# Kernel tuning notes

Hardware: AMD Instinct MI355X
Metric: run time of the kernel (lower is better)

Reference implementation:

```python
import jax, jax.numpy as jnp
import numpy as np

N_NODES = 50000
N_EDGES = 800000
N_GRAPHS = 64
IN_DIM = 128
HID = 128
S, C = 4, 16
DIM1 = 3 * S * S  # 48
OUT_DIM = DIM1 * C  # 768


def gcn_conv(x, W, b, src, dst, w):
    """PyG GCNConv: linear transform, then sym-normalized aggregation with self-loops (weight 1)."""
    n = x.shape[0]
    h = x @ W  # [N, out]
    deg = jnp.zeros((n,), x.dtype).at[dst].add(w) + 1.0  # self-loop weight 1
    dinv = jax.lax.rsqrt(deg)
    norm = dinv[src] * w * dinv[dst]  # [E]
    agg = jnp.zeros_like(h).at[dst].add(h[src] * norm[:, None])
    agg = agg + h * (1.0 / deg)[:, None]  # self-loop messages
    return agg + b


def setup_inputs() -> dict:
    key = jax.random.key(0)
    ks = jax.random.split(key, 16)
    x = jax.random.normal(ks[0], (N_NODES, IN_DIM), jnp.float32)
    edge_index = jax.random.randint(ks[1], (2, N_EDGES), 0, N_NODES, jnp.int64)
    edge_attr = jax.random.uniform(ks[2], (N_EDGES,), jnp.float32)
    batch = jnp.sort(jax.random.randint(ks[3], (N_NODES,), 0, N_GRAPHS, jnp.int64))

    def glorot(k, fan_in, fan_out):
        s = np.sqrt(6.0 / (fan_in + fan_out)).astype(np.float32)
        return jax.random.uniform(k, (fan_in, fan_out), jnp.float32, -s, s)

    return {
        "x": x, "edge_index": edge_index, "edge_attr": edge_attr, "batch": batch,
        "W1": glorot(ks[4], IN_DIM, HID), "b1": jnp.zeros((HID,), jnp.float32),
        "W2": glorot(ks[5], HID, HID // 2), "b2": jnp.zeros((HID // 2,), jnp.float32),
        "W3": glorot(ks[6], HID // 2, HID // 4), "b3": jnp.zeros((HID // 4,), jnp.float32),
        "Wl": glorot(ks[7], HID // 4, OUT_DIM), "bl": jnp.zeros((OUT_DIM,), jnp.float32),
    }


def reference(x, edge_index, edge_attr, batch, W1, b1, W2, b2, W3, b3, Wl, bl):
    src, dst = edge_index[0], edge_index[1]
    w = edge_attr / edge_attr.max()
    h = jax.nn.relu(gcn_conv(x, W1, b1, src, dst, w))
    h = jax.nn.relu(gcn_conv(h, W2, b2, src, dst, w))
    h = jax.nn.relu(gcn_conv(h, W3, b3, src, dst, w))
    # global mean pool over graphs
    sums = jax.ops.segment_sum(h, batch, num_segments=N_GRAPHS)
    cnt = jax.ops.segment_sum(jnp.ones((h.shape[0],), h.dtype), batch, num_segments=N_GRAPHS)
    pooled = sums / jnp.maximum(cnt, 1.0)[:, None]
    out = pooled @ Wl + bl  # [G, OUT_DIM]
    return out.reshape(N_GRAPHS, DIM1, C)
```

## Files before the change

### kernel.cpp

```cpp
#include <hip/hip_runtime.h>
#include <hip/hip_bf16.h>

#define NN 50000
#define NE 800000
#define NG 64
#define OUTD 768

#define G1B ((NN + 63) / 64)
#define MAXB 128
#define SSEG 64
#define TTL 8
#define ESEG (NE / SSEG)
#define NTL (NN / TTL)
#define HRB (SSEG * TTL)

__device__ __forceinline__ float bflo(unsigned int u) { return __uint_as_float(u << 16); }
__device__ __forceinline__ float bfhi(unsigned int u) { return __uint_as_float(u & 0xffff0000u); }
__device__ __forceinline__ unsigned short f2bf(float f) {
    unsigned int u = __float_as_uint(f);
    return (unsigned short)((u + 0x7fffu + ((u >> 16) & 1u)) >> 16);
}
__device__ __forceinline__ unsigned int pack2bf(float lo, float hi) {
    return (unsigned int)f2bf(lo) | ((unsigned int)f2bf(hi) << 16);
}

typedef __attribute__((ext_vector_type(8))) short bf16x8;
typedef __attribute__((ext_vector_type(4))) float f32x4;
union FragU { uint4 u4; bf16x8 v; };

template <int K, int N>
constexpr int mfma_lds_bytes() { return (K / 32) * (N / 16) * 1024; }

template <int K, int N, typename TX>
__device__ __forceinline__ void mfma_gemm_body(char* smem,
                                               const TX* __restrict__ X,
                                               const float* __restrict__ W,
                                               unsigned short* __restrict__ Y,
                                               int nRows, int bx) {
    constexpr int NCT = N / 16;
    constexpr int KS = K / 32;
    const int tid = threadIdx.x;

    for (int q = tid; q < KS * NCT * 64; q += 256) {
        int lane = q & 63;
        int fi = q >> 6;
        int ct = fi % NCT, kc = fi / NCT;
        int col = ct * 16 + (lane & 15);
        int kb = kc * 32 + ((lane >> 4) << 3);
        uint4 w;
        w.x = pack2bf(W[(size_t)(kb + 0) * N + col], W[(size_t)(kb + 1) * N + col]);
        w.y = pack2bf(W[(size_t)(kb + 2) * N + col], W[(size_t)(kb + 3) * N + col]);
        w.z = pack2bf(W[(size_t)(kb + 4) * N + col], W[(size_t)(kb + 5) * N + col]);
        w.w = pack2bf(W[(size_t)(kb + 6) * N + col], W[(size_t)(kb + 7) * N + col]);
        *(uint4*)(smem + (size_t)q * 16) = w;
    }
    __syncthreads();

    const int lane = tid & 63;
    const int wv = tid >> 6;
    const int m = lane & 15;
    const int quad = lane >> 4;
    const int row = bx * 64 + wv * 16 + m;
    const bool rowok = row < nRows;
    const TX* xr = X + (size_t)(rowok ? row : 0) * K;

    f32x4 acc[NCT];
#pragma unroll
    for (int ct = 0; ct < NCT; ++ct) acc[ct] = (f32x4){0.f, 0.f, 0.f, 0.f};

#pragma unroll
    for (int kc = 0; kc < KS; ++kc) {
        const int k0 = kc * 32 + quad * 8;
        FragU a;
        if constexpr (sizeof(TX) == 4) {
            float4 a0 = make_float4(0.f, 0.f, 0.f, 0.f), a1 = a0;
            if (rowok) {
                a0 = *(const float4*)(xr + k0);
                a1 = *(const float4*)(xr + k0 + 4);
            }
            a.u4 = make_uint4(pack2bf(a0.x, a0.y), pack2bf(a0.z, a0.w),
                              pack2bf(a1.x, a1.y), pack2bf(a1.z, a1.w));
        } else {
            a.u4 = rowok ? *(const uint4*)(xr + k0) : make_uint4(0, 0, 0, 0);
        }
#pragma unroll
        for (int ct = 0; ct < NCT; ++ct) {
            FragU b;
            b.u4 = *(const uint4*)(smem + ((size_t)(kc * NCT + ct) * 64 + lane) * 16);
            acc[ct] = __builtin_amdgcn_mfma_f32_16x16x32_bf16(a.v, b.v, acc[ct], 0, 0, 0);
        }
    }

    const int orowb = bx * 64 + wv * 16 + quad * 4;
#pragma unroll
    for (int ct = 0; ct < NCT; ++ct) {
        int col = ct * 16 + m;
#pragma unroll
        for (int r = 0; r < 4; ++r) {
            int orow = orowb + r;
            if (orow < nRows) Y[(size_t)orow * N + col] = f2bf(acc[ct][r]);
        }
    }
}

template <int K, int N, typename TX>
__global__ __launch_bounds__(256) void mfma_gemm_kernel(const TX* __restrict__ X,
                                                        const float* __restrict__ W,
                                                        unsigned short* __restrict__ Y,
                                                        int nRows) {
    extern __shared__ char smem[];
    mfma_gemm_body<K, N>(smem, X, W, Y, nRows, blockIdx.x);
}

__global__ __launch_bounds__(256) void fused1_kernel(const float* __restrict__ x,
                                                     const float* __restrict__ W1,
                                                     unsigned short* __restrict__ bufA,
                                                     const float* __restrict__ ea,
                                                     unsigned int* wmax,
                                                     const int* __restrict__ dst,
                                                     int* __restrict__ rank,
                                                     unsigned short* __restrict__ pcnt) {
    extern __shared__ char smem[];
    const int b = blockIdx.x;
    if (b < G1B) {
        mfma_gemm_body<128, 128>(smem, x, W1, bufA, NN, b);
    } else if (b < G1B + MAXB) {
        float* red = (float*)smem;
        const int bb = b - G1B;
        float m = 0.0f;
        for (int i = bb * 256 + threadIdx.x; i < NE; i += MAXB * 256)
            m = fmaxf(m, ea[i]);
        red[threadIdx.x] = m;
        __syncthreads();
        for (int off = 128; off > 0; off >>= 1) {
            if (threadIdx.x < off)
                red[threadIdx.x] = fmaxf(red[threadIdx.x], red[threadIdx.x + off]);
            __syncthreads();
        }
        if (threadIdx.x == 0) atomicMax(wmax, __float_as_uint(red[0]));
    } else {
        const int b2 = b - G1B - MAXB;
        const int seg = b2 >> 3;
        const int tile = b2 & 7;
        int* lcnt = (int*)smem;
        for (int i = threadIdx.x; i < NTL; i += 256) lcnt[i] = 0;
        __syncthreads();
        const int base = seg * ESEG;
        const int nlo = tile * NTL;
        for (int e = base + threadIdx.x; e < base + ESEG; e += 256) {
            int d = dst[e] - nlo;
            if ((unsigned)d < (unsigned)NTL)
                rank[e] = atomicAdd(&lcnt[d], 1);
        }
        __syncthreads();
        unsigned short* prow = pcnt + (size_t)seg * NN + nlo;
        for (int i = threadIdx.x; i < NTL; i += 256)
            prow[i] = (unsigned short)lcnt[i];
    }
}

__global__ __launch_bounds__(256) void comb_kernel(unsigned short* __restrict__ pcnt,
                                                   int* __restrict__ hist,
                                                   int* __restrict__ blocksum) {
    __shared__ int red[256];
    int n = blockIdx.x * 256 + threadIdx.x;
    int run = 0;
    if (n < NN) {
#pragma unroll
        for (int s = 0; s < SSEG; ++s) {
            size_t idx = (size_t)s * NN + n;
            int v = pcnt[idx];
            pcnt[idx] = (unsigned short)run;
            run += v;
        }
        hist[n] = run;
    }
    red[threadIdx.x] = (n < NN) ? run : 0;
    __syncthreads();
    for (int off = 128; off > 0; off >>= 1) {
        if (threadIdx.x < off) red[threadIdx.x] += red[threadIdx.x + off];
        __syncthreads();
    }
    if (threadIdx.x == 0) blocksum[blockIdx.x] = red[0];
}

__global__ __launch_bounds__(256) void scan2_kernel(const int* __restrict__ blocksum,
                                                    int* __restrict__ blockoff,
                                                    int* __restrict__ total_out, int nb) {
    __shared__ int s[256];
    const int tid = threadIdx.x;
    int v = (tid < nb) ? blocksum[tid] : 0;
    s[tid] = v;
    __syncthreads();
    for (int off = 1; off < 256; off <<= 1) {
        int t = (tid >= off) ? s[tid - off] : 0;
        __syncthreads();
        s[tid] += t;
        __syncthreads();
    }
    if (tid < nb) blockoff[tid] = s[tid] - v;
    if (tid == nb - 1) *total_out = s[tid];
}

__global__ __launch_bounds__(256) void scan3_kernel(const int* __restrict__ hist,
                                                    const int* __restrict__ blockoff,
                                                    int* __restrict__ rowptr, int n) {
    __shared__ int s[256];
    const int tid = threadIdx.x;
    int i = blockIdx.x * 256 + tid;
    int v = (i < n) ? hist[i] : 0;
    s[tid] = v;
    __syncthreads();
    for (int off = 1; off < 256; off <<= 1) {
        int t = (tid >= off) ? s[tid - off] : 0;
        __syncthreads();
        s[tid] += t;
        __syncthreads();
    }
    if (i < n) rowptr[i] = blockoff[blockIdx.x] + s[tid] - v;
}

__global__ void scat_kernel(const int* __restrict__ src, const int* __restrict__ dst,
                            const float* __restrict__ ea,
                            const int* __restrict__ rowptr,
                            const unsigned short* __restrict__ pcnt,
                            const int* __restrict__ rank,
                            int2* __restrict__ epack, int nE) {
    int e = blockIdx.x * blockDim.x + threadIdx.x;
    if (e >= nE) return;
    int s = e / ESEG;
    int d = dst[e];
    int pos = rowptr[d] + (int)pcnt[(size_t)s * NN + d] + rank[e];
    epack[pos] = make_int2(src[e], __float_as_int(ea[e]));
}

__global__ void deg_kernel(const int2* __restrict__ epack, const int* __restrict__ rowptr,
                           const unsigned int* __restrict__ wmax,
                           float* __restrict__ dinv, float* __restrict__ invdeg, int n) {
    int i = blockIdx.x * blockDim.x + threadIdx.x;
    if (i >= n) return;
    float rw = 1.0f / __uint_as_float(*wmax);
    int s0 = rowptr[i], s1 = rowptr[i + 1];
    float s = 0.f;
    for (int e = s0; e < s1; ++e) s += __int_as_float(epack[e].y);
    float d = fmaf(s, rw, 1.0f);
    dinv[i] = rsqrtf(d);
    invdeg[i] = 1.0f / d;
}

__global__ void coef_kernel(int2* __restrict__ epack, const int* __restrict__ rowptr,
                            const float* __restrict__ dinv,
                            const unsigned int* __restrict__ wmax, int n) {
    int i = blockIdx.x * blockDim.x + threadIdx.x;
    if (i >= n) return;
    float rw = 1.0f / __uint_as_float(*wmax);
    float di = dinv[i];
    int s0 = rowptr[i], s1 = rowptr[i + 1];
    for (int e = s0; e < s1; ++e) {
        int2 p = epack[e];
        p.y = __float_as_int(dinv[p.x] * (__int_as_float(p.y) * rw) * di);
        epack[e] = p;
    }
}

template <int D>
__global__ __launch_bounds__(256) void agg_kernel(const unsigned short* __restrict__ H,
                                                  const int* __restrict__ rowptr,
                                                  const int2* __restrict__ epack,
                                                  const float* __restrict__ invdeg,
                                                  const float* __restrict__ bias,
                                                  unsigned short* __restrict__ out,
                                                  int nNodes) {
    constexpr int LPE = D / 8;
    constexpr int EPW = 64 / LPE;
    const int lane = threadIdx.x & 63;
    const int n = (blockIdx.x << 2) | (threadIdx.x >> 6);
    if (n >= nNodes) return;
    const int esub = lane / LPE;
    const int f8 = (lane % LPE) * 8;
    const int s0 = rowptr[n];
    const int cnt = rowptr[n + 1] - s0;

    float a[8] = {};
    int kb = 0;
    for (; kb + 2 * EPW <= cnt; kb += 2 * EPW) {
        const int2 pa = epack[s0 + kb + esub];
        const int2 pb = epack[s0 + kb + EPW + esub];
        const uint4 ua = *(const uint4*)(H + (size_t)pa.x * D + f8);
        const uint4 ub = *(const uint4*)(H + (size_t)pb.x * D + f8);
        const float ca = __int_as_float(pa.y);
        const float cb = __int_as_float(pb.y);
        a[0] = fmaf(ca, bflo(ua.x), a[0]); a[1] = fmaf(ca, bfhi(ua.x), a[1]);
        a[2] = fmaf(ca, bflo(ua.y), a[2]); a[3] = fmaf(ca, bfhi(ua.y), a[3]);
        a[4] = fmaf(ca, bflo(ua.z), a[4]); a[5] = fmaf(ca, bfhi(ua.z), a[5]);
        a[6] = fmaf(ca, bflo(ua.w), a[6]); a[7] = fmaf(ca, bfhi(ua.w), a[7]);
        a[0] = fmaf(cb, bflo(ub.x), a[0]); a[1] = fmaf(cb, bfhi(ub.x), a[1]);
        a[2] = fmaf(cb, bflo(ub.y), a[2]); a[3] = fmaf(cb, bfhi(ub.y), a[3]);
        a[4] = fmaf(cb, bflo(ub.z), a[4]); a[5] = fmaf(cb, bfhi(ub.z), a[5]);
        a[6] = fmaf(cb, bflo(ub.w), a[6]); a[7] = fmaf(cb, bfhi(ub.w), a[7]);
    }
    for (; kb < cnt; kb += EPW) {
        const int idx = kb + esub;
        const bool ok = idx < cnt;
        const int2 p = ok ? epack[s0 + idx] : make_int2(n, 0);
        const uint4 u = *(const uint4*)(H + (size_t)p.x * D + f8);
        const float c = ok ? __int_as_float(p.y) : 0.f;
        a[0] = fmaf(c, bflo(u.x), a[0]); a[1] = fmaf(c, bfhi(u.x), a[1]);
        a[2] = fmaf(c, bflo(u.y), a[2]); a[3] = fmaf(c, bfhi(u.y), a[3]);
        a[4] = fmaf(c, bflo(u.z), a[4]); a[5] = fmaf(c, bfhi(u.z), a[5]);
        a[6] = fmaf(c, bflo(u.w), a[6]); a[7] = fmaf(c, bfhi(u.w), a[7]);
    }
#pragma unroll
    for (int off = LPE; off < 64; off <<= 1) {
#pragma unroll
        for (int j = 0; j < 8; ++j) a[j] += __shfl_xor(a[j], off);
    }
    if (esub == 0) {
        const float id = invdeg[n];
        const uint4 un = *(const uint4*)(H + (size_t)n * D + f8);
        const float4 b0 = *(const float4*)(bias + f8);
        const float4 b1 = *(const float4*)(bias + f8 + 4);
        float o[8];
        o[0] = fmaxf(fmaf(id, bflo(un.x), a[0]) + b0.x, 0.f);
        o[1] = fmaxf(fmaf(id, bfhi(un.x), a[1]) + b0.y, 0.f);
        o[2] = fmaxf(fmaf(id, bflo(un.y), a[2]) + b0.z, 0.f);
        o[3] = fmaxf(fmaf(id, bfhi(un.y), a[3]) + b0.w, 0.f);
        o[4] = fmaxf(fmaf(id, bflo(un.z), a[4]) + b1.x, 0.f);
        o[5] = fmaxf(fmaf(id, bfhi(un.z), a[5]) + b1.y, 0.f);
        o[6] = fmaxf(fmaf(id, bflo(un.w), a[6]) + b1.z, 0.f);
        o[7] = fmaxf(fmaf(id, bfhi(un.w), a[7]) + b1.w, 0.f);
        uint4 w;
        w.x = pack2bf(o[0], o[1]);
        w.y = pack2bf(o[2], o[3]);
        w.z = pack2bf(o[4], o[5]);
        w.w = pack2bf(o[6], o[7]);
        *(uint4*)(out + (size_t)n * D + f8) = w;
    }
}

__global__ __launch_bounds__(256) void pool2_kernel(const unsigned short* __restrict__ h,
                                                    const int* __restrict__ batch,
                                                    float* __restrict__ pooled, int n) {
    const int g = blockIdx.x;
    int lo = 0, hi = n;
    while (lo < hi) { int m = (lo + hi) >> 1; if (batch[m] < g) lo = m + 1; else hi = m; }
    const int start = lo;
    lo = start; hi = n;
    while (lo < hi) { int m = (lo + hi) >> 1; if (batch[m] < g + 1) lo = m + 1; else hi = m; }
    const int end = lo;

    __shared__ float part[256];
    const int f = threadIdx.x & 31;
    const int r = threadIdx.x >> 5;
    float acc = 0.f;
    for (int i = start + r; i < end; i += 8)
        acc += __uint_as_float((unsigned int)h[(size_t)i * 32 + f] << 16);
    part[threadIdx.x] = acc;
    __syncthreads();
    if (threadIdx.x < 32) {
        float s = 0.f;
#pragma unroll
        for (int q = 0; q < 8; ++q) s += part[q * 32 + f];
        float inv = 1.0f / fmaxf((float)(end - start), 1.0f);
        pooled[g * 32 + f] = s * inv;
    }
}

__global__ void final_kernel(const float* __restrict__ pooled,
                             const float* __restrict__ Wl, const float* __restrict__ bl,
                             float* __restrict__ out) {
    int idx = blockIdx.x * blockDim.x + threadIdx.x;
    int g = idx / OUTD, o = idx - g * OUTD;
    float acc = bl[o];
#pragma unroll
    for (int k = 0; k < 32; ++k)
        acc = fmaf(pooled[g * 32 + k], Wl[k * OUTD + o], acc);
    out[idx] = acc;
}

extern "C" void kernel_launch(void* const* d_in, const int* in_sizes, int n_in,
                              void* d_out, int out_size, void* d_ws, size_t ws_size,
                              hipStream_t stream) {
    const float* x = (const float*)d_in[0];
    const int* eidx = (const int*)d_in[1];
    const float* ea = (const float*)d_in[2];
    const int* batch = (const int*)d_in[3];
    const float* W1 = (const float*)d_in[4];
    const float* b1 = (const float*)d_in[5];
    const float* W2 = (const float*)d_in[6];
    const float* b2 = (const float*)d_in[7];
    const float* W3 = (const float*)d_in[8];
    const float* b3 = (const float*)d_in[9];
    const float* Wl = (const float*)d_in[10];
    const float* bl = (const float*)d_in[11];
    const int* src = eidx;
    const int* dst = eidx + NE;

    char* p = (char*)d_ws;
    auto take = [&](size_t bytes) {
        char* r = p;
        p += (bytes + 255) & ~(size_t)255;
        return r;
    };
    float* dinv = (float*)take(NN * 4);
    float* invdeg = (float*)take(NN * 4);
    int* hist = (int*)take(NN * 4);
    int* rowptr = (int*)take((NN + 1) * 4);
    int* blocksum = (int*)take(256 * 4);
    int* blockoff = (int*)take(256 * 4);
    int2* epack = (int2*)take((size_t)NE * 8);
    float* pooled = (float*)take(NG * 32 * 4);
    unsigned int* wmax = (unsigned int*)take(4);
    unsigned short* bufA = (unsigned short*)take((size_t)NN * 128 * 2);
    unsigned short* bufB = (unsigned short*)take((size_t)NN * 128 * 2);
    int* rank = (int*)bufB;
    unsigned short* pcnt = (unsigned short*)((char*)bufB + (size_t)NE * 4 + 256);

    const int nblk = (NN + 255) / 256;
    const int eblk = (NE + 255) / 256;

    hipMemsetAsync(wmax, 0, 4, stream);

    constexpr int LDS1 = mfma_lds_bytes<128, 128>();
    static_assert(LDS1 >= NTL * 4, "HR branch LDS must fit");
    fused1_kernel<<<G1B + MAXB + HRB, 256, LDS1, stream>>>(x, W1, bufA, ea, wmax,
                                                           dst, rank, pcnt);
    comb_kernel<<<nblk, 256, 0, stream>>>(pcnt, hist, blocksum);
    scan2_kernel<<<1, 256, 0, stream>>>(blocksum, blockoff, &rowptr[NN], nblk);
    scan3_kernel<<<nblk, 256, 0, stream>>>(hist, blockoff, rowptr, NN);
    scat_kernel<<<eblk, 256, 0, stream>>>(src, dst, ea, rowptr, pcnt, rank, epack, NE);
    deg_kernel<<<nblk, 256, 0, stream>>>(epack, rowptr, wmax, dinv, invdeg, NN);
    coef_kernel<<<nblk, 256, 0, stream>>>(epack, rowptr, dinv, wmax, NN);

    agg_kernel<128><<<(NN + 3) / 4, 256, 0, stream>>>(bufA, rowptr, epack, invdeg, b1, bufB, NN);
    mfma_gemm_kernel<128, 64, unsigned short>
        <<<G1B, 256, mfma_lds_bytes<128, 64>(), stream>>>(bufB, W2, bufA, NN);
    agg_kernel<64><<<(NN + 3) / 4, 256, 0, stream>>>(bufA, rowptr, epack, invdeg, b2, bufB, NN);
    mfma_gemm_kernel<64, 32, unsigned short>
        <<<G1B, 256, mfma_lds_bytes<64, 32>(), stream>>>(bufB, W3, bufA, NN);
    agg_kernel<32><<<(NN + 7) / 8 * 2, 256, 0, stream>>>(bufA, rowptr, epack, invdeg, b3, bufB, NN);

    pool2_kernel<<<NG, 256, 0, stream>>>(bufB, batch, pooled, NN);
    final_kernel<<<(NG * OUTD) / 256, 256, 0, stream>>>(pooled, Wl, bl, (float*)d_out);
}
```

Baseline: 294.0 us.

## Fuse CSR-build kernels with grid barriers and prepack weight fragments once

Merges the comb, scan, scatter, degree and coefficient kernels into one persistent kernel of 196 blocks, with atomic grid-wide barriers between phases, to cut launch overhead. Weight fragments are pre-converted to bf16 MFMA layout in a separate prep kernel, and the GEMMs read them from global memory instead of rebuilding them in LDS per block. Histogram counters are packed two 16-bit values per 32-bit LDS word, so tiles per segment drop from 8 to 4. The grid barrier relies on all 196 blocks being co-resident, and the agg<32> launch grid also changes.

```diff
diff --git a/kernel.cpp b/kernel.cpp
--- a/kernel.cpp
+++ b/kernel.cpp
@@ -7,12 +7,18 @@
 #define OUTD 768
 
 #define G1B ((NN + 63) / 64)
-#define MAXB 128
 #define SSEG 64
-#define TTL 8
+#define TTL 4
 #define ESEG (NE / SSEG)
 #define NTL (NN / TTL)
 #define HRB (SSEG * TTL)
+#define WB 16
+#define MAXB 128
+#define NB 196
+
+#define W1E 2048
+#define W2E 1024
+#define W3E 256
 
 __device__ __forceinline__ float bflo(unsigned int u) { return __uint_as_float(u << 16); }
 __device__ __forceinline__ float bfhi(unsigned int u) { return __uint_as_float(u & 0xffff0000u); }
@@ -28,34 +34,57 @@
 typedef __attribute__((ext_vector_type(4))) float f32x4;
 union FragU { uint4 u4; bf16x8 v; };
 
-template <int K, int N>
-constexpr int mfma_lds_bytes() { return (K / 32) * (N / 16) * 1024; }
+__global__ __launch_bounds__(256) void prep_kernel(const float* __restrict__ W1,
+                                                   const float* __restrict__ W2,
+                                                   const float* __restrict__ W3,
+                                                   uint4* __restrict__ f1,
+                                                   uint4* __restrict__ f2,
+                                                   uint4* __restrict__ f3,
+                                                   const float* __restrict__ ea,
+                                                   unsigned int* wmax) {
+    const int b = blockIdx.x;
+    if (b < WB) {
+        for (int q = b * 256 + threadIdx.x; q < W1E + W2E + W3E; q += WB * 256) {
+            const float* W; uint4* F; int N, qq;
+            if (q < W1E) { W = W1; F = f1; N = 128; qq = q; }
+            else if (q < W1E + W2E) { W = W2; F = f2; N = 64; qq = q - W1E; }
+            else { W = W3; F = f3; N = 32; qq = q - W1E - W2E; }
+            int lane = qq & 63, fi = qq >> 6;
+            int NCT = N / 16, ct = fi % NCT, kc = fi / NCT;
+            int col = ct * 16 + (lane & 15);
+            int kb = kc * 32 + ((lane >> 4) << 3);
+            uint4 w;
+            w.x = pack2bf(W[(size_t)(kb + 0) * N + col], W[(size_t)(kb + 1) * N + col]);
+            w.y = pack2bf(W[(size_t)(kb + 2) * N + col], W[(size_t)(kb + 3) * N + col]);
+            w.z = pack2bf(W[(size_t)(kb + 4) * N + col], W[(size_t)(kb + 5) * N + col]);
+            w.w = pack2bf(W[(size_t)(kb + 6) * N + col], W[(size_t)(kb + 7) * N + col]);
+            F[qq] = w;
+        }
+    } else {
+        __shared__ float red[256];
+        const int bb = b - WB;
+        float m = 0.0f;
+        for (int i = bb * 256 + threadIdx.x; i < NE; i += MAXB * 256)
+            m = fmaxf(m, ea[i]);
+        red[threadIdx.x] = m;
+        __syncthreads();
+        for (int off = 128; off > 0; off >>= 1) {
+            if (threadIdx.x < off)
+                red[threadIdx.x] = fmaxf(red[threadIdx.x], red[threadIdx.x + off]);
+            __syncthreads();
+        }
+        if (threadIdx.x == 0) atomicMax(wmax, __float_as_uint(red[0]));
+    }
+}
 
 template <int K, int N, typename TX>
-__device__ __forceinline__ void mfma_gemm_body(char* smem,
-                                               const TX* __restrict__ X,
-                                               const float* __restrict__ W,
-                                               unsigned short* __restrict__ Y,
-                                               int nRows, int bx) {
+__device__ __forceinline__ void mfma_gemm_tbl(const TX* __restrict__ X,
+                                              const uint4* __restrict__ ftab,
+                                              unsigned short* __restrict__ Y,
+                                              int nRows, int bx) {
     constexpr int NCT = N / 16;
     constexpr int KS = K / 32;
     const int tid = threadIdx.x;
-
-    for (int q = tid; q < KS * NCT * 64; q += 256) {
-        int lane = q & 63;
-        int fi = q >> 6;
-        int ct = fi % NCT, kc = fi / NCT;
-        int col = ct * 16 + (lane & 15);
-        int kb = kc * 32 + ((lane >> 4) << 3);
-        uint4 w;
-        w.x = pack2bf(W[(size_t)(kb + 0) * N + col], W[(size_t)(kb + 1) * N + col]);
-        w.y = pack2bf(W[(size_t)(kb + 2) * N + col], W[(size_t)(kb + 3) * N + col]);
-        w.z = pack2bf(W[(size_t)(kb + 4) * N + col], W[(size_t)(kb + 5) * N + col]);
-        w.w = pack2bf(W[(size_t)(kb + 6) * N + col], W[(size_t)(kb + 7) * N + col]);
-        *(uint4*)(smem + (size_t)q * 16) = w;
-    }
-    __syncthreads();
-
     const int lane = tid & 63;
     const int wv = tid >> 6;
     const int m = lane & 15;
@@ -86,7 +115,7 @@
 #pragma unroll
         for (int ct = 0; ct < NCT; ++ct) {
             FragU b;
-            b.u4 = *(const uint4*)(smem + ((size_t)(kc * NCT + ct) * 64 + lane) * 16);
+            b.u4 = ftab[(kc * NCT + ct) * 64 + lane];
             acc[ct] = __builtin_amdgcn_mfma_f32_16x16x32_bf16(a.v, b.v, acc[ct], 0, 0, 0);
         }
     }
@@ -105,65 +134,71 @@
 
 template <int K, int N, typename TX>
 __global__ __launch_bounds__(256) void mfma_gemm_kernel(const TX* __restrict__ X,
-                                                        const float* __restrict__ W,
+                                                        const uint4* __restrict__ ftab,
                                                         unsigned short* __restrict__ Y,
                                                         int nRows) {
-    extern __shared__ char smem[];
-    mfma_gemm_body<K, N>(smem, X, W, Y, nRows, blockIdx.x);
+    mfma_gemm_tbl<K, N>(X, ftab, Y, nRows, blockIdx.x);
 }
 
 __global__ __launch_bounds__(256) void fused1_kernel(const float* __restrict__ x,
-                                                     const float* __restrict__ W1,
+                                                     const uint4* __restrict__ f1,
                                                      unsigned short* __restrict__ bufA,
-                                                     const float* __restrict__ ea,
-                                                     unsigned int* wmax,
                                                      const int* __restrict__ dst,
                                                      int* __restrict__ rank,
                                                      unsigned short* __restrict__ pcnt) {
-    extern __shared__ char smem[];
+    extern __shared__ unsigned int lcnt[];
     const int b = blockIdx.x;
     if (b < G1B) {
-        mfma_gemm_body<128, 128>(smem, x, W1, bufA, NN, b);
-    } else if (b < G1B + MAXB) {
-        float* red = (float*)smem;
-        const int bb = b - G1B;
-        float m = 0.0f;
-        for (int i = bb * 256 + threadIdx.x; i < NE; i += MAXB * 256)
-            m = fmaxf(m, ea[i]);
-        red[threadIdx.x] = m;
-        __syncthreads();
-        for (int off = 128; off > 0; off >>= 1) {
-            if (threadIdx.x < off)
-                red[threadIdx.x] = fmaxf(red[threadIdx.x], red[threadIdx.x + off]);
-            __syncthreads();
-        }
-        if (threadIdx.x == 0) atomicMax(wmax, __float_as_uint(red[0]));
+        mfma_gemm_tbl<128, 128>(x, f1, bufA, NN, b);
     } else {
-        const int b2 = b - G1B - MAXB;
-        const int seg = b2 >> 3;
-        const int tile = b2 & 7;
-        int* lcnt = (int*)smem;
-        for (int i = threadIdx.x; i < NTL; i += 256) lcnt[i] = 0;
+        const int b2 = b - G1B;
+        const int seg = b2 >> 2;
+        const int tile = b2 & 3;
+        for (int i = threadIdx.x; i < NTL / 2; i += 256) lcnt[i] = 0;
         __syncthreads();
         const int base = seg * ESEG;
         const int nlo = tile * NTL;
         for (int e = base + threadIdx.x; e < base + ESEG; e += 256) {
             int d = dst[e] - nlo;
-            if ((unsigned)d < (unsigned)NTL)
-                rank[e] = atomicAdd(&lcnt[d], 1);
-        }
-        __syncthreads();
-        unsigned short* prow = pcnt + (size_t)seg * NN + nlo;
-        for (int i = threadIdx.x; i < NTL; i += 256)
-            prow[i] = (unsigned short)lcnt[i];
-    }
-}
-
-__global__ __launch_bounds__(256) void comb_kernel(unsigned short* __restrict__ pcnt,
-                                                   int* __restrict__ hist,
-                                                   int* __restrict__ blocksum) {
-    __shared__ int red[256];
-    int n = blockIdx.x * 256 + threadIdx.x;
+            if ((unsigned)d < (unsigned)NTL) {
+                unsigned int add = (d & 1) ? 0x10000u : 1u;
+                unsigned int old = atomicAdd(&lcnt[d >> 1], add);
+                rank[e] = (int)((old >> ((d & 1) * 16)) & 0xffffu);
+            }
+        }
+        __syncthreads();
+        unsigned int* prow32 = (unsigned int*)(pcnt + (size_t)seg * NN + nlo);
+        for (int i = threadIdx.x; i < NTL / 2; i += 256) prow32[i] = lcnt[i];
+    }
+}
+
+__device__ __forceinline__ void gridbar(unsigned int* bar, unsigned int target) {
+    __syncthreads();
+    if (threadIdx.x == 0) {
+        __hip_atomic_fetch_add(bar, 1u, __ATOMIC_ACQ_REL, __HIP_MEMORY_SCOPE_AGENT);
+        while (__hip_atomic_load(bar, __ATOMIC_ACQUIRE, __HIP_MEMORY_SCOPE_AGENT) < target)
+            __builtin_amdgcn_s_sleep(2);
+    }
+    __syncthreads();
+}
+
+__global__ __launch_bounds__(256) void mid_kernel(unsigned short* __restrict__ pcnt,
+                                                  int* __restrict__ rowptr,
+                                                  int* __restrict__ blocksum,
+                                                  const int* __restrict__ src,
+                                                  const int* __restrict__ dst,
+                                                  const float* __restrict__ ea,
+                                                  const int* __restrict__ rank,
+                                                  int2* __restrict__ epack,
+                                                  const unsigned int* __restrict__ wmax,
+                                                  float* __restrict__ dinv,
+                                                  float* __restrict__ invdeg,
+                                                  unsigned int* bar) {
+    __shared__ int sh[256];
+    const int tid = threadIdx.x;
+    const int b = blockIdx.x;
+    const int n = b * 256 + tid;
+
     int run = 0;
     if (n < NN) {
 #pragma unroll
@@ -173,93 +208,67 @@
             pcnt[idx] = (unsigned short)run;
             run += v;
         }
-        hist[n] = run;
-    }
-    red[threadIdx.x] = (n < NN) ? run : 0;
+    }
+    sh[tid] = run;
     __syncthreads();
     for (int off = 128; off > 0; off >>= 1) {
-        if (threadIdx.x < off) red[threadIdx.x] += red[threadIdx.x + off];
-        __syncthreads();
-    }
-    if (threadIdx.x == 0) blocksum[blockIdx.x] = red[0];
-}
-
-__global__ __launch_bounds__(256) void scan2_kernel(const int* __restrict__ blocksum,
-                                                    int* __restrict__ blockoff,
-                                                    int* __restrict__ total_out, int nb) {
-    __shared__ int s[256];
-    const int tid = threadIdx.x;
-    int v = (tid < nb) ? blocksum[tid] : 0;
-    s[tid] = v;
+        if (tid < off) sh[tid] += sh[tid + off];
+        __syncthreads();
+    }
+    if (tid == 0) blocksum[b] = sh[0];
+    gridbar(bar, NB);
+
+    int v2 = (tid < NB) ? blocksum[tid] : 0;
+    __syncthreads();
+    sh[tid] = v2;
     __syncthreads();
     for (int off = 1; off < 256; off <<= 1) {
-        int t = (tid >= off) ? s[tid - off] : 0;
-        __syncthreads();
-        s[tid] += t;
-        __syncthreads();
-    }
-    if (tid < nb) blockoff[tid] = s[tid] - v;
-    if (tid == nb - 1) *total_out = s[tid];
-}
-
-__global__ __launch_bounds__(256) void scan3_kernel(const int* __restrict__ hist,
-                                                    const int* __restrict__ blockoff,
-                                                    int* __restrict__ rowptr, int n) {
-    __shared__ int s[256];
-    const int tid = threadIdx.x;
-    int i = blockIdx.x * 256 + tid;
-    int v = (i < n) ? hist[i] : 0;
-    s[tid] = v;
+        int t = (tid >= off) ? sh[tid - off] : 0;
+        __syncthreads();
+        sh[tid] += t;
+        __syncthreads();
+    }
+    const int blockoff = (b > 0) ? sh[b - 1] : 0;
+    if (b == 0 && tid == 0) rowptr[NN] = sh[NB - 1];
+    __syncthreads();
+    sh[tid] = run;
     __syncthreads();
     for (int off = 1; off < 256; off <<= 1) {
-        int t = (tid >= off) ? s[tid - off] : 0;
-        __syncthreads();
-        s[tid] += t;
-        __syncthreads();
-    }
-    if (i < n) rowptr[i] = blockoff[blockIdx.x] + s[tid] - v;
-}
-
-__global__ void scat_kernel(const int* __restrict__ src, const int* __restrict__ dst,
-                            const float* __restrict__ ea,
-                            const int* __restrict__ rowptr,
-                            const unsigned short* __restrict__ pcnt,
-                            const int* __restrict__ rank,
-                            int2* __restrict__ epack, int nE) {
-    int e = blockIdx.x * blockDim.x + threadIdx.x;
-    if (e >= nE) return;
-    int s = e / ESEG;
-    int d = dst[e];
-    int pos = rowptr[d] + (int)pcnt[(size_t)s * NN + d] + rank[e];
-    epack[pos] = make_int2(src[e], __float_as_int(ea[e]));
-}
-
-__global__ void deg_kernel(const int2* __restrict__ epack, const int* __restrict__ rowptr,
-                           const unsigned int* __restrict__ wmax,
-                           float* __restrict__ dinv, float* __restrict__ invdeg, int n) {
-    int i = blockIdx.x * blockDim.x + threadIdx.x;
-    if (i >= n) return;
-    float rw = 1.0f / __uint_as_float(*wmax);
-    int s0 = rowptr[i], s1 = rowptr[i + 1];
-    float s = 0.f;
-    for (int e = s0; e < s1; ++e) s += __int_as_float(epack[e].y);
-    float d = fmaf(s, rw, 1.0f);
-    dinv[i] = rsqrtf(d);
-    invdeg[i] = 1.0f / d;
-}
-
-__global__ void coef_kernel(int2* __restrict__ epack, const int* __restrict__ rowptr,
-                            const float* __restrict__ dinv,
-                            const unsigned int* __restrict__ wmax, int n) {
-    int i = blockIdx.x * blockDim.x + threadIdx.x;
-    if (i >= n) return;
-    float rw = 1.0f / __uint_as_float(*wmax);
-    float di = dinv[i];
-    int s0 = rowptr[i], s1 = rowptr[i + 1];
-    for (int e = s0; e < s1; ++e) {
-        int2 p = epack[e];
-        p.y = __float_as_int(dinv[p.x] * (__int_as_float(p.y) * rw) * di);
-        epack[e] = p;
+        int t = (tid >= off) ? sh[tid - off] : 0;
+        __syncthreads();
+        sh[tid] += t;
+        __syncthreads();
+    }
+    if (n < NN) rowptr[n] = blockoff + sh[tid] - run;
+    gridbar(bar, 2 * NB);
+
+    for (int e = b * 256 + tid; e < NE; e += NB * 256) {
+        int s = e / ESEG;
+        int d = dst[e];
+        int pos = rowptr[d] + (int)pcnt[(size_t)s * NN + d] + rank[e];
+        epack[pos] = make_int2(src[e], __float_as_int(ea[e]));
+    }
+    gridbar(bar, 3 * NB);
+
+    const float rw = 1.0f / __uint_as_float(*wmax);
+    if (n < NN) {
+        int s0 = rowptr[n], s1 = rowptr[n + 1];
+        float s = 0.f;
+        for (int e = s0; e < s1; ++e) s += __int_as_float(epack[e].y);
+        float d = fmaf(s, rw, 1.0f);
+        dinv[n] = rsqrtf(d);
+        invdeg[n] = 1.0f / d;
+    }
+    gridbar(bar, 4 * NB);
+
+    if (n < NN) {
+        float di = dinv[n];
+        int s0 = rowptr[n], s1 = rowptr[n + 1];
+        for (int e = s0; e < s1; ++e) {
+            int2 p = epack[e];
+            p.y = __float_as_int(dinv[p.x] * (__int_as_float(p.y) * rw) * di);
+            epack[e] = p;
+        }
     }
 }
 
@@ -404,41 +413,34 @@
     };
     float* dinv = (float*)take(NN * 4);
     float* invdeg = (float*)take(NN * 4);
-    int* hist = (int*)take(NN * 4);
     int* rowptr = (int*)take((NN + 1) * 4);
     int* blocksum = (int*)take(256 * 4);
-    int* blockoff = (int*)take(256 * 4);
     int2* epack = (int2*)take((size_t)NE * 8);
     float* pooled = (float*)take(NG * 32 * 4);
-    unsigned int* wmax = (unsigned int*)take(4);
+    unsigned int* wmaxbar = (unsigned int*)take(8);
+    uint4* f1 = (uint4*)take(W1E * 16);
+    uint4* f2 = (uint4*)take(W2E * 16);
+    uint4* f3 = (uint4*)take(W3E * 16);
     unsigned short* bufA = (unsigned short*)take((size_t)NN * 128 * 2);
     unsigned short* bufB = (unsigned short*)take((size_t)NN * 128 * 2);
     int* rank = (int*)bufB;
     unsigned short* pcnt = (unsigned short*)((char*)bufB + (size_t)NE * 4 + 256);
 
-    const int nblk = (NN + 255) / 256;
-    const int eblk = (NE + 255) / 256;
-
-    hipMemsetAsync(wmax, 0, 4, stream);
-
-    constexpr int LDS1 = mfma_lds_bytes<128, 128>();
-    static_assert(LDS1 >= NTL * 4, "HR branch LDS must fit");
-    fused1_kernel<<<G1B + MAXB + HRB, 256, LDS1, stream>>>(x, W1, bufA, ea, wmax,
-                                                           dst, rank, pcnt);
-    comb_kernel<<<nblk, 256, 0, stream>>>(pcnt, hist, blocksum);
-    scan2_kernel<<<1, 256, 0, stream>>>(blocksum, blockoff, &rowptr[NN], nblk);
-    scan3_kernel<<<nblk, 256, 0, stream>>>(hist, blockoff, rowptr, NN);
-    scat_kernel<<<eblk, 256, 0, stream>>>(src, dst, ea, rowptr, pcnt, rank, epack, NE);
-    deg_kernel<<<nblk, 256, 0, stream>>>(epack, rowptr, wmax, dinv, invdeg, NN);
-    coef_kernel<<<nblk, 256, 0, stream>>>(epack, rowptr, dinv, wmax, NN);
+    unsigned int* wmax = wmaxbar;
+    unsigned int* bar = wmaxbar + 1;
+
+    hipMemsetAsync(wmaxbar, 0, 8, stream);
+
+    prep_kernel<<<WB + MAXB, 256, 0, stream>>>(W1, W2, W3, f1, f2, f3, ea, wmax);
+    fused1_kernel<<<G1B + HRB, 256, (NTL / 2) * 4, stream>>>(x, f1, bufA, dst, rank, pcnt);
+    mid_kernel<<<NB, 256, 0, stream>>>(pcnt, rowptr, blocksum, src, dst, ea, rank,
+                                       epack, wmax, dinv, invdeg, bar);
 
     agg_kernel<128><<<(NN + 3) / 4, 256, 0, stream>>>(bufA, rowptr, epack, invdeg, b1, bufB, NN);
-    mfma_gemm_kernel<128, 64, unsigned short>
-        <<<G1B, 256, mfma_lds_bytes<128, 64>(), stream>>>(bufB, W2, bufA, NN);
+    mfma_gemm_kernel<128, 64, unsigned short><<<G1B, 256, 0, stream>>>(bufB, f2, bufA, NN);
     agg_kernel<64><<<(NN + 3) / 4, 256, 0, stream>>>(bufA, rowptr, epack, invdeg, b2, bufB, NN);
-    mfma_gemm_kernel<64, 32, unsigned short>
-        <<<G1B, 256, mfma_lds_bytes<64, 32>(), stream>>>(bufB, W3, bufA, NN);
-    agg_kernel<32><<<(NN + 7) / 8 * 2, 256, 0, stream>>>(bufA, rowptr, epack, invdeg, b3, bufB, NN);
+    mfma_gemm_kernel<64, 32, unsigned short><<<G1B, 256, 0, stream>>>(bufB, f3, bufA, NN);
+    agg_kernel<32><<<(NN + 3) / 4, 256, 0, stream>>>(bufA, rowptr, epack, invdeg, b3, bufB, NN);
 
     pool2_kernel<<<NG, 256, 0, stream>>>(bufB, batch, pooled, NN);
     final_kernel<<<(NG * OUTD) / 256, 256, 0, stream>>>(pooled, Wl, bl, (float*)d_out);
```

Result: slower. 350.7 us (+19.3%).

## Pre-pack weight fragments once and pack 16-bit histogram counters in LDS

Applied to the files above, without the earlier changes.

A new prep kernel converts W1/W2/W3 into bf16 MFMA fragment tables in global memory once, and also does the edge-weight max reduction. The GEMM blocks then read B fragments straight from that table instead of each block restaging and converting the weights into LDS behind a barrier. The dst histogram now packs two 16-bit counters per 32-bit LDS word, so 4 node tiles fit instead of 8 and fewer edge-scan blocks are needed. The agg<32> grid also changes. This adds an extra launch and relies on per-segment counts staying below 65536, which holds for 12500 edges per segment.

```diff
diff --git a/kernel.cpp b/kernel.cpp
--- a/kernel.cpp
+++ b/kernel.cpp
@@ -7,12 +7,17 @@
 #define OUTD 768
 
 #define G1B ((NN + 63) / 64)
-#define MAXB 128
 #define SSEG 64
-#define TTL 8
+#define TTL 4
 #define ESEG (NE / SSEG)
 #define NTL (NN / TTL)
 #define HRB (SSEG * TTL)
+#define WB 16
+#define MAXB 128
+
+#define W1E 2048
+#define W2E 1024
+#define W3E 256
 
 __device__ __forceinline__ float bflo(unsigned int u) { return __uint_as_float(u << 16); }
 __device__ __forceinline__ float bfhi(unsigned int u) { return __uint_as_float(u & 0xffff0000u); }
@@ -28,34 +33,57 @@
 typedef __attribute__((ext_vector_type(4))) float f32x4;
 union FragU { uint4 u4; bf16x8 v; };
 
-template <int K, int N>
-constexpr int mfma_lds_bytes() { return (K / 32) * (N / 16) * 1024; }
+__global__ __launch_bounds__(256) void prep_kernel(const float* __restrict__ W1,
+                                                   const float* __restrict__ W2,
+                                                   const float* __restrict__ W3,
+                                                   uint4* __restrict__ f1,
+                                                   uint4* __restrict__ f2,
+                                                   uint4* __restrict__ f3,
+                                                   const float* __restrict__ ea,
+                                                   unsigned int* wmax) {
+    const int b = blockIdx.x;
+    if (b < WB) {
+        for (int q = b * 256 + threadIdx.x; q < W1E + W2E + W3E; q += WB * 256) {
+            const float* W; uint4* F; int N, qq;
+            if (q < W1E) { W = W1; F = f1; N = 128; qq = q; }
+            else if (q < W1E + W2E) { W = W2; F = f2; N = 64; qq = q - W1E; }
+            else { W = W3; F = f3; N = 32; qq = q - W1E - W2E; }
+            int lane = qq & 63, fi = qq >> 6;
+            int NCT = N / 16, ct = fi % NCT, kc = fi / NCT;
+            int col = ct * 16 + (lane & 15);
+            int kb = kc * 32 + ((lane >> 4) << 3);
+            uint4 w;
+            w.x = pack2bf(W[(size_t)(kb + 0) * N + col], W[(size_t)(kb + 1) * N + col]);
+            w.y = pack2bf(W[(size_t)(kb + 2) * N + col], W[(size_t)(kb + 3) * N + col]);
+            w.z = pack2bf(W[(size_t)(kb + 4) * N + col], W[(size_t)(kb + 5) * N + col]);
+            w.w = pack2bf(W[(size_t)(kb + 6) * N + col], W[(size_t)(kb + 7) * N + col]);
+            F[qq] = w;
+        }
+    } else {
+        __shared__ float red[256];
+        const int bb = b - WB;
+        float m = 0.0f;
+        for (int i = bb * 256 + threadIdx.x; i < NE; i += MAXB * 256)
+            m = fmaxf(m, ea[i]);
+        red[threadIdx.x] = m;
+        __syncthreads();
+        for (int off = 128; off > 0; off >>= 1) {
+            if (threadIdx.x < off)
+                red[threadIdx.x] = fmaxf(red[threadIdx.x], red[threadIdx.x + off]);
+            __syncthreads();
+        }
+        if (threadIdx.x == 0) atomicMax(wmax, __float_as_uint(red[0]));
+    }
+}
 
 template <int K, int N, typename TX>
-__device__ __forceinline__ void mfma_gemm_body(char* smem,
-                                               const TX* __restrict__ X,
-                                               const float* __restrict__ W,
-                                               unsigned short* __restrict__ Y,
-                                               int nRows, int bx) {
+__device__ __forceinline__ void mfma_gemm_tbl(const TX* __restrict__ X,
+                                              const uint4* __restrict__ ftab,
+                                              unsigned short* __restrict__ Y,
+                                              int nRows, int bx) {
     constexpr int NCT = N / 16;
     constexpr int KS = K / 32;
     const int tid = threadIdx.x;
-
-    for (int q = tid; q < KS * NCT * 64; q += 256) {
-        int lane = q & 63;
-        int fi = q >> 6;
-        int ct = fi % NCT, kc = fi / NCT;
-        int col = ct * 16 + (lane & 15);
-        int kb = kc * 32 + ((lane >> 4) << 3);
-        uint4 w;
-        w.x = pack2bf(W[(size_t)(kb + 0) * N + col], W[(size_t)(kb + 1) * N + col]);
-        w.y = pack2bf(W[(size_t)(kb + 2) * N + col], W[(size_t)(kb + 3) * N + col]);
-        w.z = pack2bf(W[(size_t)(kb + 4) * N + col], W[(size_t)(kb + 5) * N + col]);
-        w.w = pack2bf(W[(size_t)(kb + 6) * N + col], W[(size_t)(kb + 7) * N + col]);
-        *(uint4*)(smem + (size_t)q * 16) = w;
-    }
-    __syncthreads();
-
     const int lane = tid & 63;
     const int wv = tid >> 6;
     const int m = lane & 15;
@@ -86,7 +114,7 @@
 #pragma unroll
         for (int ct = 0; ct < NCT; ++ct) {
             FragU b;
-            b.u4 = *(const uint4*)(smem + ((size_t)(kc * NCT + ct) * 64 + lane) * 16);
+            b.u4 = ftab[(kc * NCT + ct) * 64 + lane];
             acc[ct] = __builtin_amdgcn_mfma_f32_16x16x32_bf16(a.v, b.v, acc[ct], 0, 0, 0);
         }
     }
@@ -105,57 +133,41 @@
 
 template <int K, int N, typename TX>
 __global__ __launch_bounds__(256) void mfma_gemm_kernel(const TX* __restrict__ X,
-                                                        const float* __restrict__ W,
+                                                        const uint4* __restrict__ ftab,
                                                         unsigned short* __restrict__ Y,
                                                         int nRows) {
-    extern __shared__ char smem[];
-    mfma_gemm_body<K, N>(smem, X, W, Y, nRows, blockIdx.x);
+    mfma_gemm_tbl<K, N>(X, ftab, Y, nRows, blockIdx.x);
 }
 
 __global__ __launch_bounds__(256) void fused1_kernel(const float* __restrict__ x,
-                                                     const float* __restrict__ W1,
+                                                     const uint4* __restrict__ f1,
                                                      unsigned short* __restrict__ bufA,
-                                                     const float* __restrict__ ea,
-                                                     unsigned int* wmax,
                                                      const int* __restrict__ dst,
                                                      int* __restrict__ rank,
                                                      unsigned short* __restrict__ pcnt) {
-    extern __shared__ char smem[];
+    extern __shared__ unsigned int lcnt[];
     const int b = blockIdx.x;
     if (b < G1B) {
-        mfma_gemm_body<128, 128>(smem, x, W1, bufA, NN, b);
-    } else if (b < G1B + MAXB) {
-        float* red = (float*)smem;
-        const int bb = b - G1B;
-        float m = 0.0f;
-        for (int i = bb * 256 + threadIdx.x; i < NE; i += MAXB * 256)
-            m = fmaxf(m, ea[i]);
-        red[threadIdx.x] = m;
-        __syncthreads();
-        for (int off = 128; off > 0; off >>= 1) {
-            if (threadIdx.x < off)
-                red[threadIdx.x] = fmaxf(red[threadIdx.x], red[threadIdx.x + off]);
-            __syncthreads();
-        }
-        if (threadIdx.x == 0) atomicMax(wmax, __float_as_uint(red[0]));
+        mfma_gemm_tbl<128, 128>(x, f1, bufA, NN, b);
     } else {
-        const int b2 = b - G1B - MAXB;
-        const int seg = b2 >> 3;
-        const int tile = b2 & 7;
-        int* lcnt = (int*)smem;
-        for (int i = threadIdx.x; i < NTL; i += 256) lcnt[i] = 0;
+        const int b2 = b - G1B;
+        const int seg = b2 >> 2;
+        const int tile = b2 & 3;
+        for (int i = threadIdx.x; i < NTL / 2; i += 256) lcnt[i] = 0;
         __syncthreads();
         const int base = seg * ESEG;
         const int nlo = tile * NTL;
         for (int e = base + threadIdx.x; e < base + ESEG; e += 256) {
             int d = dst[e] - nlo;
-            if ((unsigned)d < (unsigned)NTL)
-                rank[e] = atomicAdd(&lcnt[d], 1);
-        }
-        __syncthreads();
-        unsigned short* prow = pcnt + (size_t)seg * NN + nlo;
-        for (int i = threadIdx.x; i < NTL; i += 256)
-            prow[i] = (unsigned short)lcnt[i];
+            if ((unsigned)d < (unsigned)NTL) {
+                unsigned int add = (d & 1) ? 0x10000u : 1u;
+                unsigned int old = atomicAdd(&lcnt[d >> 1], add);
+                rank[e] = (int)((old >> ((d & 1) * 16)) & 0xffffu);
+            }
+        }
+        __syncthreads();
+        unsigned int* prow32 = (unsigned int*)(pcnt + (size_t)seg * NN + nlo);
+        for (int i = threadIdx.x; i < NTL / 2; i += 256) prow32[i] = lcnt[i];
     }
 }
 
@@ -411,6 +423,9 @@
     int2* epack = (int2*)take((size_t)NE * 8);
     float* pooled = (float*)take(NG * 32 * 4);
     unsigned int* wmax = (unsigned int*)take(4);
+    uint4* f1 = (uint4*)take(W1E * 16);
+    uint4* f2 = (uint4*)take(W2E * 16);
+    uint4* f3 = (uint4*)take(W3E * 16);
     unsigned short* bufA = (unsigned short*)take((size_t)NN * 128 * 2);
     unsigned short* bufB = (unsigned short*)take((size_t)NN * 128 * 2);
     int* rank = (int*)bufB;
@@ -421,10 +436,8 @@
 
     hipMemsetAsync(wmax, 0, 4, stream);
 
-    constexpr int LDS1 = mfma_lds_bytes<128, 128>();
-    static_assert(LDS1 >= NTL * 4, "HR branch LDS must fit");
-    fused1_kernel<<<G1B + MAXB + HRB, 256, LDS1, stream>>>(x, W1, bufA, ea, wmax,
-                                                           dst, rank, pcnt);
+    prep_kernel<<<WB + MAXB, 256, 0, stream>>>(W1, W2, W3, f1, f2, f3, ea, wmax);
+    fused1_kernel<<<G1B + HRB, 256, (NTL / 2) * 4, stream>>>(x, f1, bufA, dst, rank, pcnt);
     comb_kernel<<<nblk, 256, 0, stream>>>(pcnt, hist, blocksum);
     scan2_kernel<<<1, 256, 0, stream>>>(blocksum, blockoff, &rowptr[NN], nblk);
     scan3_kernel<<<nblk, 256, 0, stream>>>(hist, blockoff, rowptr, NN);
@@ -433,12 +446,10 @@
     coef_kernel<<<nblk, 256, 0, stream>>>(epack, rowptr, dinv, wmax, NN);
 
     agg_kernel<128><<<(NN + 3) / 4, 256, 0, stream>>>(bufA, rowptr, epack, invdeg, b1, bufB, NN);
-    mfma_gemm_kernel<128, 64, unsigned short>
-        <<<G1B, 256, mfma_lds_bytes<128, 64>(), stream>>>(bufB, W2, bufA, NN);
+    mfma_gemm_kernel<128, 64, unsigned short><<<G1B, 256, 0, stream>>>(bufB, f2, bufA, NN);
     agg_kernel<64><<<(NN + 3) / 4, 256, 0, stream>>>(bufA, rowptr, epack, invdeg, b2, bufB, NN);
-    mfma_gemm_kernel<64, 32, unsigned short>
-        <<<G1B, 256, mfma_lds_bytes<64, 32>(), stream>>>(bufB, W3, bufA, NN);
-    agg_kernel<32><<<(NN + 7) / 8 * 2, 256, 0, stream>>>(bufA, rowptr, epack, invdeg, b3, bufB, NN);
+    mfma_gemm_kernel<64, 32, unsigned short><<<G1B, 256, 0, stream>>>(bufB, f3, bufA, NN);
+    agg_kernel<32><<<(NN + 3) / 4, 256, 0, stream>>>(bufA, rowptr, epack, invdeg, b3, bufB, NN);
 
     pool2_kernel<<<NG, 256, 0, stream>>>(bufB, batch, pooled, NN);
     final_kernel<<<(NG * OUTD) / 256, 256, 0, stream>>>(pooled, Wl, bl, (float*)d_out);
```

After: 301.4 us. 1.02x slower.

## Fuse scan, degree/coef and pool/final kernels using software grid barriers

Applied to the files above, without the earlier changes.

Merges the three-kernel row-pointer scan into one kernel that uses an atomic spin grid barrier across 196 co-resident blocks. The degree and coefficient passes are merged the same way. The weight normalisation moves into the scatter kernel, inverse degree is recomputed as dinv squared, and pooling is fused with the final linear layer. The goal is to cut kernel launches and small intermediate buffers, but correctness now depends on all barrier blocks being resident at once. The launch grid of the last aggregation also changes.

```diff
diff --git a/kernel.cpp b/kernel.cpp
--- a/kernel.cpp
+++ b/kernel.cpp
@@ -13,6 +13,7 @@
 #define ESEG (NE / SSEG)
 #define NTL (NN / TTL)
 #define HRB (SSEG * TTL)
+#define NB 196
 
 __device__ __forceinline__ float bflo(unsigned int u) { return __uint_as_float(u << 16); }
 __device__ __forceinline__ float bfhi(unsigned int u) { return __uint_as_float(u & 0xffff0000u); }
@@ -159,11 +160,25 @@
     }
 }
 
-__global__ __launch_bounds__(256) void comb_kernel(unsigned short* __restrict__ pcnt,
-                                                   int* __restrict__ hist,
-                                                   int* __restrict__ blocksum) {
-    __shared__ int red[256];
-    int n = blockIdx.x * 256 + threadIdx.x;
+__device__ __forceinline__ void gridbar(unsigned int* bar, unsigned int target) {
+    __syncthreads();
+    if (threadIdx.x == 0) {
+        __hip_atomic_fetch_add(bar, 1u, __ATOMIC_ACQ_REL, __HIP_MEMORY_SCOPE_AGENT);
+        while (__hip_atomic_load(bar, __ATOMIC_ACQUIRE, __HIP_MEMORY_SCOPE_AGENT) < target)
+            __builtin_amdgcn_s_sleep(2);
+    }
+    __syncthreads();
+}
+
+__global__ __launch_bounds__(256) void comb_scan_kernel(unsigned short* __restrict__ pcnt,
+                                                        int* __restrict__ rowptr,
+                                                        int* __restrict__ blocksum,
+                                                        unsigned int* bar) {
+    __shared__ int sh[256];
+    const int tid = threadIdx.x;
+    const int b = blockIdx.x;
+    const int n = b * 256 + tid;
+
     int run = 0;
     if (n < NN) {
 #pragma unroll
@@ -173,51 +188,38 @@
             pcnt[idx] = (unsigned short)run;
             run += v;
         }
-        hist[n] = run;
-    }
-    red[threadIdx.x] = (n < NN) ? run : 0;
+    }
+    sh[tid] = run;
     __syncthreads();
     for (int off = 128; off > 0; off >>= 1) {
-        if (threadIdx.x < off) red[threadIdx.x] += red[threadIdx.x + off];
-        __syncthreads();
-    }
-    if (threadIdx.x == 0) blocksum[blockIdx.x] = red[0];
-}
-
-__global__ __launch_bounds__(256) void scan2_kernel(const int* __restrict__ blocksum,
-                                                    int* __restrict__ blockoff,
-                                                    int* __restrict__ total_out, int nb) {
-    __shared__ int s[256];
-    const int tid = threadIdx.x;
-    int v = (tid < nb) ? blocksum[tid] : 0;
-    s[tid] = v;
+        if (tid < off) sh[tid] += sh[tid + off];
+        __syncthreads();
+    }
+    if (tid == 0) blocksum[b] = sh[0];
+    gridbar(bar, NB);
+
+    int v2 = (tid < NB) ? blocksum[tid] : 0;
+    __syncthreads();
+    sh[tid] = v2;
     __syncthreads();
     for (int off = 1; off < 256; off <<= 1) {
-        int t = (tid >= off) ? s[tid - off] : 0;
-        __syncthreads();
-        s[tid] += t;
-        __syncthreads();
-    }
-    if (tid < nb) blockoff[tid] = s[tid] - v;
-    if (tid == nb - 1) *total_out = s[tid];
-}
-
-__global__ __launch_bounds__(256) void scan3_kernel(const int* __restrict__ hist,
-                                                    const int* __restrict__ blockoff,
-                                                    int* __restrict__ rowptr, int n) {
-    __shared__ int s[256];
-    const int tid = threadIdx.x;
-    int i = blockIdx.x * 256 + tid;
-    int v = (i < n) ? hist[i] : 0;
-    s[tid] = v;
+        int t = (tid >= off) ? sh[tid - off] : 0;
+        __syncthreads();
+        sh[tid] += t;
+        __syncthreads();
+    }
+    const int blockoff = (b > 0) ? sh[b - 1] : 0;
+    if (b == 0 && tid == 0) rowptr[NN] = sh[NB - 1];
+    __syncthreads();
+    sh[tid] = run;
     __syncthreads();
     for (int off = 1; off < 256; off <<= 1) {
-        int t = (tid >= off) ? s[tid - off] : 0;
-        __syncthreads();
-        s[tid] += t;
-        __syncthreads();
-    }
-    if (i < n) rowptr[i] = blockoff[blockIdx.x] + s[tid] - v;
+        int t = (tid >= off) ? sh[tid - off] : 0;
+        __syncthreads();
+        sh[tid] += t;
+        __syncthreads();
+    }
+    if (n < NN) rowptr[n] = blockoff + sh[tid] - run;
 }
 
 __global__ void scat_kernel(const int* __restrict__ src, const int* __restrict__ dst,
@@ -225,41 +227,37 @@
                             const int* __restrict__ rowptr,
                             const unsigned short* __restrict__ pcnt,
                             const int* __restrict__ rank,
+                            const unsigned int* __restrict__ wmax,
                             int2* __restrict__ epack, int nE) {
     int e = blockIdx.x * blockDim.x + threadIdx.x;
     if (e >= nE) return;
+    float rw = 1.0f / __uint_as_float(*wmax);
     int s = e / ESEG;
     int d = dst[e];
     int pos = rowptr[d] + (int)pcnt[(size_t)s * NN + d] + rank[e];
-    epack[pos] = make_int2(src[e], __float_as_int(ea[e]));
-}
-
-__global__ void deg_kernel(const int2* __restrict__ epack, const int* __restrict__ rowptr,
-                           const unsigned int* __restrict__ wmax,
-                           float* __restrict__ dinv, float* __restrict__ invdeg, int n) {
-    int i = blockIdx.x * blockDim.x + threadIdx.x;
-    if (i >= n) return;
-    float rw = 1.0f / __uint_as_float(*wmax);
-    int s0 = rowptr[i], s1 = rowptr[i + 1];
-    float s = 0.f;
-    for (int e = s0; e < s1; ++e) s += __int_as_float(epack[e].y);
-    float d = fmaf(s, rw, 1.0f);
-    dinv[i] = rsqrtf(d);
-    invdeg[i] = 1.0f / d;
-}
-
-__global__ void coef_kernel(int2* __restrict__ epack, const int* __restrict__ rowptr,
-                            const float* __restrict__ dinv,
-                            const unsigned int* __restrict__ wmax, int n) {
-    int i = blockIdx.x * blockDim.x + threadIdx.x;
-    if (i >= n) return;
-    float rw = 1.0f / __uint_as_float(*wmax);
-    float di = dinv[i];
-    int s0 = rowptr[i], s1 = rowptr[i + 1];
-    for (int e = s0; e < s1; ++e) {
-        int2 p = epack[e];
-        p.y = __float_as_int(dinv[p.x] * (__int_as_float(p.y) * rw) * di);
-        epack[e] = p;
+    epack[pos] = make_int2(src[e], __float_as_int(ea[e] * rw));
+}
+
+__global__ __launch_bounds__(256) void degcoef_kernel(int2* __restrict__ epack,
+                                                      const int* __restrict__ rowptr,
+                                                      float* __restrict__ dinv,
+                                                      unsigned int* bar) {
+    const int n = blockIdx.x * 256 + threadIdx.x;
+    int s0 = 0, s1 = 0;
+    if (n < NN) {
+        s0 = rowptr[n]; s1 = rowptr[n + 1];
+        float s = 1.0f;
+        for (int e = s0; e < s1; ++e) s += __int_as_float(epack[e].y);
+        dinv[n] = rsqrtf(s);
+    }
+    gridbar(bar, NB);
+    if (n < NN) {
+        const float di = dinv[n];
+        for (int e = s0; e < s1; ++e) {
+            int2 p = epack[e];
+            p.y = __float_as_int(dinv[p.x] * __int_as_float(p.y) * di);
+            epack[e] = p;
+        }
     }
 }
 
@@ -267,7 +265,7 @@
 __global__ __launch_bounds__(256) void agg_kernel(const unsigned short* __restrict__ H,
                                                   const int* __restrict__ rowptr,
                                                   const int2* __restrict__ epack,
-                                                  const float* __restrict__ invdeg,
+                                                  const float* __restrict__ dinv,
                                                   const float* __restrict__ bias,
                                                   unsigned short* __restrict__ out,
                                                   int nNodes) {
@@ -316,7 +314,8 @@
         for (int j = 0; j < 8; ++j) a[j] += __shfl_xor(a[j], off);
     }
     if (esub == 0) {
-        const float id = invdeg[n];
+        const float di = dinv[n];
+        const float id = di * di;
         const uint4 un = *(const uint4*)(H + (size_t)n * D + f8);
         const float4 b0 = *(const float4*)(bias + f8);
         const float4 b1 = *(const float4*)(bias + f8 + 4);
@@ -338,9 +337,11 @@
     }
 }
 
-__global__ __launch_bounds__(256) void pool2_kernel(const unsigned short* __restrict__ h,
-                                                    const int* __restrict__ batch,
-                                                    float* __restrict__ pooled, int n) {
+__global__ __launch_bounds__(256) void poolfinal_kernel(const unsigned short* __restrict__ h,
+                                                        const int* __restrict__ batch,
+                                                        const float* __restrict__ Wl,
+                                                        const float* __restrict__ bl,
+                                                        float* __restrict__ out, int n) {
     const int g = blockIdx.x;
     int lo = 0, hi = n;
     while (lo < hi) { int m = (lo + hi) >> 1; if (batch[m] < g) lo = m + 1; else hi = m; }
@@ -350,6 +351,7 @@
     const int end = lo;
 
     __shared__ float part[256];
+    __shared__ float pooled[32];
     const int f = threadIdx.x & 31;
     const int r = threadIdx.x >> 5;
     float acc = 0.f;
@@ -362,20 +364,15 @@
 #pragma unroll
         for (int q = 0; q < 8; ++q) s += part[q * 32 + f];
         float inv = 1.0f / fmaxf((float)(end - start), 1.0f);
-        pooled[g * 32 + f] = s * inv;
-    }
-}
-
-__global__ void final_kernel(const float* __restrict__ pooled,
-                             const float* __restrict__ Wl, const float* __restrict__ bl,
-                             float* __restrict__ out) {
-    int idx = blockIdx.x * blockDim.x + threadIdx.x;
-    int g = idx / OUTD, o = idx - g * OUTD;
-    float acc = bl[o];
-#pragma unroll
-    for (int k = 0; k < 32; ++k)
-        acc = fmaf(pooled[g * 32 + k], Wl[k * OUTD + o], acc);
-    out[idx] = acc;
+        pooled[f] = s * inv;
+    }
+    __syncthreads();
+    for (int o = threadIdx.x; o < OUTD; o += 256) {
+        float a = bl[o];
+#pragma unroll
+        for (int k = 0; k < 32; ++k) a = fmaf(pooled[k], Wl[k * OUTD + o], a);
+        out[(size_t)g * OUTD + o] = a;
+    }
 }
 
 extern "C" void kernel_launch(void* const* d_in, const int* in_sizes, int n_in,
@@ -403,43 +400,38 @@
         return r;
     };
     float* dinv = (float*)take(NN * 4);
-    float* invdeg = (float*)take(NN * 4);
-    int* hist = (int*)take(NN * 4);
     int* rowptr = (int*)take((NN + 1) * 4);
     int* blocksum = (int*)take(256 * 4);
-    int* blockoff = (int*)take(256 * 4);
     int2* epack = (int2*)take((size_t)NE * 8);
-    float* pooled = (float*)take(NG * 32 * 4);
-    unsigned int* wmax = (unsigned int*)take(4);
+    unsigned int* wmaxbar = (unsigned int*)take(12);
     unsigned short* bufA = (unsigned short*)take((size_t)NN * 128 * 2);
     unsigned short* bufB = (unsigned short*)take((size_t)NN * 128 * 2);
     int* rank = (int*)bufB;
     unsigned short* pcnt = (unsigned short*)((char*)bufB + (size_t)NE * 4 + 256);
 
-    const int nblk = (NN + 255) / 256;
+    unsigned int* wmax = wmaxbar;
+    unsigned int* bar1 = wmaxbar + 1;
+    unsigned int* bar2 = wmaxbar + 2;
+
     const int eblk = (NE + 255) / 256;
 
-    hipMemsetAsync(wmax, 0, 4, stream);
+    hipMemsetAsync(wmaxbar, 0, 12, stream);
 
     constexpr int LDS1 = mfma_lds_bytes<128, 128>();
     static_assert(LDS1 >= NTL * 4, "HR branch LDS must fit");
     fused1_kernel<<<G1B + MAXB + HRB, 256, LDS1, stream>>>(x, W1, bufA, ea, wmax,
                                                            dst, rank, pcnt);
-    comb_kernel<<<nblk, 256, 0, stream>>>(pcnt, hist, blocksum);
-    scan2_kernel<<<1, 256, 0, stream>>>(blocksum, blockoff, &rowptr[NN], nblk);
-    scan3_kernel<<<nblk, 256, 0, stream>>>(hist, blockoff, rowptr, NN);
-    scat_kernel<<<eblk, 256, 0, stream>>>(src, dst, ea, rowptr, pcnt, rank, epack, NE);
-    deg_kernel<<<nblk, 256, 0, stream>>>(epack, rowptr, wmax, dinv, invdeg, NN);
-    coef_kernel<<<nblk, 256, 0, stream>>>(epack, rowptr, dinv, wmax, NN);
-
-    agg_kernel<128><<<(NN + 3) / 4, 256, 0, stream>>>(bufA, rowptr, epack, invdeg, b1, bufB, NN);
+    comb_scan_kernel<<<NB, 256, 0, stream>>>(pcnt, rowptr, blocksum, bar1);
+    scat_kernel<<<eblk, 256, 0, stream>>>(src, dst, ea, rowptr, pcnt, rank, wmax, epack, NE);
+    degcoef_kernel<<<NB, 256, 0, stream>>>(epack, rowptr, dinv, bar2);
+
+    agg_kernel<128><<<(NN + 3) / 4, 256, 0, stream>>>(bufA, rowptr, epack, dinv, b1, bufB, NN);
     mfma_gemm_kernel<128, 64, unsigned short>
         <<<G1B, 256, mfma_lds_bytes<128, 64>(), stream>>>(bufB, W2, bufA, NN);
-    agg_kernel<64><<<(NN + 3) / 4, 256, 0, stream>>>(bufA, rowptr, epack, invdeg, b2, bufB, NN);
+    agg_kernel<64><<<(NN + 3) / 4, 256, 0, stream>>>(bufA, rowptr, epack, dinv, b2, bufB, NN);
     mfma_gemm_kernel<64, 32, unsigned short>
         <<<G1B, 256, mfma_lds_bytes<64, 32>(), stream>>>(bufB, W3, bufA, NN);
-    agg_kernel<32><<<(NN + 7) / 8 * 2, 256, 0, stream>>>(bufA, rowptr, epack, invdeg, b3, bufB, NN);
-
-    pool2_kernel<<<NG, 256, 0, stream>>>(bufB, batch, pooled, NN);
-    final_kernel<<<(NG * OUTD) / 256, 256, 0, stream>>>(pooled, Wl, bl, (float*)d_out);
-}
+    agg_kernel<32><<<(NN + 3) / 4, 256, 0, stream>>>(bufA, rowptr, epack, dinv, b3, bufB, NN);
+
+    poolfinal_kernel<<<NG, 256, 0, stream>>>(bufB, batch, Wl, bl, (float*)d_out, NN);
+}
```

Result: slower. 312.3 us (+6.2%).
